# Kernel tuning notes

Measured on AMD Instinct MI355X. Metric: run time of the kernel, lower is better.

Reference implementation:

```python
import jax, jax.numpy as jnp
import numpy as np

CH = 8       # MASK_HEAD.HEAD_CHANNELS
IN_CH = 8    # MASK_BRANCH.OUT_CHANNELS
MASK_OUT_STRIDE = 4
SOI = jnp.array([64.0, 128.0, 256.0, 512.0, 1024.0], dtype=jnp.float32)


def _upsample_ac(x, factor, axis):
    # align_corners=True bilinear upsample along one axis: L -> factor*(L-1)+1
    L = x.shape[axis]
    M = factor * (L - 1) + 1
    pos = jnp.arange(M, dtype=jnp.float32) / factor
    i0 = jnp.floor(pos).astype(jnp.int32)
    i1 = jnp.minimum(i0 + 1, L - 1)
    frac = pos - i0.astype(jnp.float32)
    x0 = jnp.take(x, i0, axis=axis)
    x1 = jnp.take(x, i1, axis=axis)
    sh = [1] * x.ndim
    sh[axis] = M
    frac = frac.reshape(sh)
    return x0 * (1.0 - frac) + x1 * frac


def aligned_bilinear(x, factor):
    # x: [n, 1, H, W] -> [n, 1, factor*H, factor*W] (AdelaiDet aligned_bilinear)
    if factor == 1:
        return x
    h, w = x.shape[2], x.shape[3]
    x = jnp.pad(x, ((0, 0), (0, 0), (0, 1), (0, 1)), mode='edge')
    x = _upsample_ac(x, factor, 2)
    x = _upsample_ac(x, factor, 3)
    p = factor // 2
    x = jnp.pad(x, ((0, 0), (0, 0), (p, 0), (p, 0)), mode='edge')
    return x[:, :, :factor * h, :factor * w]


def setup_inputs() -> dict:
    key = jax.random.key(0)
    k1, k2, k3, k4, k5, k6 = jax.random.split(key, 6)
    N, H, W = 4, 128, 128
    n_inst = 400
    num_gen = (IN_CH + 2) * CH + CH + CH * CH + CH + CH * 1 + 1  # 169
    return {
        'mask_feats': jax.random.normal(k1, (N, IN_CH, H, W), dtype=jnp.float32),
        'mask_shift': jax.random.uniform(k2, (H * W, 2), dtype=jnp.float32),
        'shifts': jax.random.uniform(k3, (n_inst, 2), dtype=jnp.float32),
        'inst_params': jax.random.normal(k4, (n_inst, num_gen), dtype=jnp.float32),
        'im_inds': jax.random.randint(k5, (n_inst,), 0, N, dtype=jnp.int32),
        'fpn_levels': jax.random.randint(k6, (n_inst,), 0, 5, dtype=jnp.int32),
        'mask_feat_stride': 8,
    }


def reference(mask_feats, mask_shift, shifts, inst_params, im_inds, fpn_levels, mask_feat_stride):
    n = inst_params.shape[0]
    N, C, H, W = mask_feats.shape
    # relative coords: [n, 2, H*W]
    rel = shifts[:, None, :] - mask_shift[None, :, :]          # [n, HW, 2]
    rel = jnp.transpose(rel, (0, 2, 1))                        # [n, 2, HW]
    rel = rel / SOI[fpn_levels][:, None, None]
    feats = mask_feats[im_inds].reshape(n, C, H * W)           # [n, C, HW]
    x = jnp.concatenate([rel, feats], axis=1)                  # [n, C+2, HW]
    # parse dynamic params: weights first, then biases
    w1 = inst_params[:, 0:80].reshape(n, CH, IN_CH + 2)
    w2 = inst_params[:, 80:144].reshape(n, CH, CH)
    w3 = inst_params[:, 144:152].reshape(n, 1, CH)
    b1 = inst_params[:, 152:160]
    b2 = inst_params[:, 160:168]
    b3 = inst_params[:, 168:169]
    # per-instance 1x1 convs == batched tiny GEMMs
    x = jax.nn.relu(jnp.einsum('noc,ncp->nop', w1, x) + b1[:, :, None])
    x = jax.nn.relu(jnp.einsum('noc,ncp->nop', w2, x) + b2[:, :, None])
    x = jnp.einsum('noc,ncp->nop', w3, x) + b3[:, :, None]
    logits = x.reshape(n, 1, H, W)
    factor = int(mask_feat_stride) // MASK_OUT_STRIDE
    return aligned_bilinear(logits, factor)
```

## Files before the change

### kernel.cpp

```cpp
#include <hip/hip_runtime.h>


#define HW 16384
#define NP 169

__global__ __launch_bounds__(256)
void pack_kernel(const float* __restrict__ mf, float* __restrict__ rec)
{
    const int g   = blockIdx.x * 256 + threadIdx.x;
    const int img = g >> 14;
    const int p   = g & 16383;
    const float* fb = mf + (size_t)img * 8 * HW + p;
    float4 a = make_float4(fb[0],      fb[HW],     fb[2 * HW], fb[3 * HW]);
    float4 b = make_float4(fb[4 * HW], fb[5 * HW], fb[6 * HW], fb[7 * HW]);
    float4* o = (float4*)(rec + (size_t)g * 8);
    o[0] = a;
    o[1] = b;
}

__global__ __launch_bounds__(256, 6)
void dmh_kernel(const float* __restrict__ mask_feats,
                const float* __restrict__ mask_shift,
                const float* __restrict__ shifts,
                const float* __restrict__ inst_params,
                const int*   __restrict__ im_inds,
                const int*   __restrict__ fpn_levels,
                const float* __restrict__ rec,
                float*       __restrict__ out,
                int use_rec)
{
    __shared__ float lgE[17 * 64];
    __shared__ float lgO[17 * 64];

    const int bx   = blockIdx.x;
    const int inst = bx >> 3;
    const int rg   = bx & 7;
    const int tid  = threadIdx.x;
    const int r0   = rg * 16;

    const int img = im_inds[inst];
    const float* __restrict__ wp = inst_params + (size_t)inst * NP;
    const float s0  = shifts[2 * inst];
    const float s1  = shifts[2 * inst + 1];
    const float inv = 1.0f / (float)(64 << fpn_levels[inst]);
    const float* __restrict__ fb = mask_feats + (size_t)img * 8 * HW;
    const float* __restrict__ rb = rec + (size_t)img * 8 * HW;

    auto load_px = [&](int p, float* x) {
        const int t = p >> 7;
        const int c = p & 127;
        const int r = min(max(r0 - 1 + t, 0), 127);
        const int g = r * 128 + c;
        const float2 ms = *(const float2*)(mask_shift + 2 * g);
        x[0] = (s0 - ms.x) * inv;
        x[1] = (s1 - ms.y) * inv;
        if (use_rec) {
            const float4* q = (const float4*)(rb + (size_t)g * 8);
            const float4 a = q[0], b = q[1];
            x[2] = a.x; x[3] = a.y; x[4] = a.z; x[5] = a.w;
            x[6] = b.x; x[7] = b.y; x[8] = b.z; x[9] = b.w;
        } else {
            #pragma unroll
            for (int k = 0; k < 8; ++k) x[2 + k] = fb[k * HW + g];
        }
    };

    auto store_px = [&](int p, float v) {
        const int t = p >> 7;
        const int c = p & 127;
        const int idx = t * 64 + (c >> 1);
        if (c & 1) lgO[idx] = v; else lgE[idx] = v;
    };

    #pragma unroll
    for (int u = 0; u < 4; ++u) {
        const int pA = tid + 512 * u;
        const int pB = pA + 256;
        float xa[10], xb[10];
        load_px(pA, xa);
        load_px(pB, xb);

        float ya[8], yb[8];
        #pragma unroll
        for (int o = 0; o < 8; ++o) {
            const float bia = wp[152 + o];
            float a = bia, b = bia;
            #pragma unroll
            for (int c = 0; c < 10; ++c) {
                const float w = wp[o * 10 + c];
                a = fmaf(w, xa[c], a);
                b = fmaf(w, xb[c], b);
            }
            ya[o] = fmaxf(a, 0.f);
            yb[o] = fmaxf(b, 0.f);
        }
        float za[8], zb[8];
        #pragma unroll
        for (int o = 0; o < 8; ++o) {
            const float bia = wp[160 + o];
            float a = bia, b = bia;
            #pragma unroll
            for (int c = 0; c < 8; ++c) {
                const float w = wp[80 + o * 8 + c];
                a = fmaf(w, ya[c], a);
                b = fmaf(w, yb[c], b);
            }
            za[o] = fmaxf(a, 0.f);
            zb[o] = fmaxf(b, 0.f);
        }
        float va = wp[168], vb = va;
        #pragma unroll
        for (int c = 0; c < 8; ++c) {
            const float w = wp[144 + c];
            va = fmaf(w, za[c], va);
            vb = fmaf(w, zb[c], vb);
        }
        store_px(pA, va);
        store_px(pB, vb);
    }

    if (tid < 128) {
        const int p = 2048 + tid;
        float x[10];
        load_px(p, x);
        float y1[8];
        #pragma unroll
        for (int o = 0; o < 8; ++o) {
            float a = wp[152 + o];
            #pragma unroll
            for (int c = 0; c < 10; ++c) a = fmaf(wp[o * 10 + c], x[c], a);
            y1[o] = fmaxf(a, 0.f);
        }
        float y2[8];
        #pragma unroll
        for (int o = 0; o < 8; ++o) {
            float a = wp[160 + o];
            #pragma unroll
            for (int c = 0; c < 8; ++c) a = fmaf(wp[80 + o * 8 + c], y1[c], a);
            y2[o] = fmaxf(a, 0.f);
        }
        float v = wp[168];
        #pragma unroll
        for (int c = 0; c < 8; ++c) v = fmaf(wp[144 + c], y2[c], v);
        store_px(p, v);
    }

    __syncthreads();

    float* __restrict__ op =
        out + (size_t)inst * 65536 + (size_t)(2 * r0) * 256;
    const int w = tid >> 6;
    const int l = tid & 63;
    const int parity = w & 1;

    #pragma unroll
    for (int j = 0; j < 8; ++j) {
        const int p2 = (w >> 1) + 2 * j;
        const int yl = 2 * p2 + parity;
        float4 res;
        if (parity) {
            const float* e = lgE + (p2 + 1) * 64;
            const float* o = lgO + (p2 + 1) * 64;
            const float v0 = e[l];
            const float v1 = o[l];
            const float vm = (l > 0) ? o[l - 1] : v0;
            res = make_float4(0.5f * (vm + v0), v0, 0.5f * (v0 + v1), v1);
        } else {
            const float* eA = lgE + p2 * 64;
            const float* oA = lgO + p2 * 64;
            const float* eB = eA + 64;
            const float* oB = oA + 64;
            const float v0A = eA[l], v1A = oA[l];
            const float v0B = eB[l], v1B = oB[l];
            const float vmA = (l > 0) ? oA[l - 1] : v0A;
            const float vmB = (l > 0) ? oB[l - 1] : v0B;
            res = make_float4(0.25f * (vmA + v0A + vmB + v0B),
                              0.5f  * (v0A + v0B),
                              0.25f * (v0A + v1A + v0B + v1B),
                              0.5f  * (v1A + v1B));
        }
        *(float4*)(op + yl * 256 + 4 * l) = res;
    }
}

extern "C" void kernel_launch(void* const* d_in, const int* in_sizes, int n_in,
                              void* d_out, int out_size, void* d_ws, size_t ws_size,
                              hipStream_t stream) {
    (void)n_in; (void)out_size;
    const float* mask_feats  = (const float*)d_in[0];
    const float* mask_shift  = (const float*)d_in[1];
    const float* shifts      = (const float*)d_in[2];
    const float* inst_params = (const float*)d_in[3];
    const int*   im_inds     = (const int*)d_in[4];
    const int*   fpn_levels  = (const int*)d_in[5];
    float* out = (float*)d_out;
    float* rec = (float*)d_ws;

    const int n_inst = in_sizes[2] / 2;
    const size_t rec_bytes = (size_t)4 * HW * 8 * sizeof(float);
    const int use_rec = (ws_size >= rec_bytes) ? 1 : 0;

    if (use_rec)
        pack_kernel<<<dim3(4 * HW / 256), dim3(256), 0, stream>>>(
            mask_feats, rec);

    dmh_kernel<<<dim3(n_inst * 8), dim3(256), 0, stream>>>(
        mask_feats, mask_shift, shifts, inst_params, im_inds, fpn_levels,
        rec, out, use_rec);
}
```

Measured before the change: 152.4 us.

## Drop channel-packing pre-pass and double rows per block to cut halo recompute

Removes the separate pack kernel that reorganised mask features into per-pixel records, so the main kernel reads the channel-planar layout directly with coalesced strided loads. Each block now processes 32 output rows instead of 16, which halves the block count and cuts the duplicated halo-row computation across neighbouring blocks. The trade-off is larger shared memory per block and fewer, longer blocks, which may lower occupancy or load balance. The loop is now only partially unrolled.

```diff
diff --git a/kernel.cpp b/kernel.cpp
--- a/kernel.cpp
+++ b/kernel.cpp
@@ -3,20 +3,6 @@
 
 #define HW 16384
 #define NP 169
-
-__global__ __launch_bounds__(256)
-void pack_kernel(const float* __restrict__ mf, float* __restrict__ rec)
-{
-    const int g   = blockIdx.x * 256 + threadIdx.x;
-    const int img = g >> 14;
-    const int p   = g & 16383;
-    const float* fb = mf + (size_t)img * 8 * HW + p;
-    float4 a = make_float4(fb[0],      fb[HW],     fb[2 * HW], fb[3 * HW]);
-    float4 b = make_float4(fb[4 * HW], fb[5 * HW], fb[6 * HW], fb[7 * HW]);
-    float4* o = (float4*)(rec + (size_t)g * 8);
-    o[0] = a;
-    o[1] = b;
-}
 
 __global__ __launch_bounds__(256, 6)
 void dmh_kernel(const float* __restrict__ mask_feats,
@@ -25,18 +11,16 @@
                 const float* __restrict__ inst_params,
                 const int*   __restrict__ im_inds,
                 const int*   __restrict__ fpn_levels,
-                const float* __restrict__ rec,
-                float*       __restrict__ out,
-                int use_rec)
+                float*       __restrict__ out)
 {
-    __shared__ float lgE[17 * 64];
-    __shared__ float lgO[17 * 64];
+    __shared__ float lgE[33 * 64];
+    __shared__ float lgO[33 * 64];
 
     const int bx   = blockIdx.x;
-    const int inst = bx >> 3;
-    const int rg   = bx & 7;
+    const int inst = bx >> 2;
+    const int rg   = bx & 3;
     const int tid  = threadIdx.x;
-    const int r0   = rg * 16;
+    const int r0   = rg * 32;
 
     const int img = im_inds[inst];
     const float* __restrict__ wp = inst_params + (size_t)inst * NP;
@@ -44,7 +28,6 @@
     const float s1  = shifts[2 * inst + 1];
     const float inv = 1.0f / (float)(64 << fpn_levels[inst]);
     const float* __restrict__ fb = mask_feats + (size_t)img * 8 * HW;
-    const float* __restrict__ rb = rec + (size_t)img * 8 * HW;
 
     auto load_px = [&](int p, float* x) {
         const int t = p >> 7;
@@ -54,15 +37,8 @@
         const float2 ms = *(const float2*)(mask_shift + 2 * g);
         x[0] = (s0 - ms.x) * inv;
         x[1] = (s1 - ms.y) * inv;
-        if (use_rec) {
-            const float4* q = (const float4*)(rb + (size_t)g * 8);
-            const float4 a = q[0], b = q[1];
-            x[2] = a.x; x[3] = a.y; x[4] = a.z; x[5] = a.w;
-            x[6] = b.x; x[7] = b.y; x[8] = b.z; x[9] = b.w;
-        } else {
-            #pragma unroll
-            for (int k = 0; k < 8; ++k) x[2 + k] = fb[k * HW + g];
-        }
+        #pragma unroll
+        for (int k = 0; k < 8; ++k) x[2 + k] = fb[k * HW + g];
     };
 
     auto store_px = [&](int p, float v) {
@@ -72,8 +48,8 @@
         if (c & 1) lgO[idx] = v; else lgE[idx] = v;
     };
 
-    #pragma unroll
-    for (int u = 0; u < 4; ++u) {
+    #pragma unroll 4
+    for (int u = 0; u < 8; ++u) {
         const int pA = tid + 512 * u;
         const int pB = pA + 256;
         float xa[10], xb[10];
@@ -120,7 +96,7 @@
     }
 
     if (tid < 128) {
-        const int p = 2048 + tid;
+        const int p = 4096 + tid;
         float x[10];
         load_px(p, x);
         float y1[8];
@@ -154,7 +130,7 @@
     const int parity = w & 1;
 
     #pragma unroll
-    for (int j = 0; j < 8; ++j) {
+    for (int j = 0; j < 16; ++j) {
         const int p2 = (w >> 1) + 2 * j;
         const int yl = 2 * p2 + parity;
         float4 res;
@@ -186,7 +162,7 @@
 extern "C" void kernel_launch(void* const* d_in, const int* in_sizes, int n_in,
                               void* d_out, int out_size, void* d_ws, size_t ws_size,
                               hipStream_t stream) {
-    (void)n_in; (void)out_size;
+    (void)n_in; (void)out_size; (void)d_ws; (void)ws_size;
     const float* mask_feats  = (const float*)d_in[0];
     const float* mask_shift  = (const float*)d_in[1];
     const float* shifts      = (const float*)d_in[2];
@@ -194,17 +170,10 @@
     const int*   im_inds     = (const int*)d_in[4];
     const int*   fpn_levels  = (const int*)d_in[5];
     float* out = (float*)d_out;
-    float* rec = (float*)d_ws;
 
     const int n_inst = in_sizes[2] / 2;
-    const size_t rec_bytes = (size_t)4 * HW * 8 * sizeof(float);
-    const int use_rec = (ws_size >= rec_bytes) ? 1 : 0;
 
-    if (use_rec)
-        pack_kernel<<<dim3(4 * HW / 256), dim3(256), 0, stream>>>(
-            mask_feats, rec);
-
-    dmh_kernel<<<dim3(n_inst * 8), dim3(256), 0, stream>>>(
+    dmh_kernel<<<dim3(n_inst * 4), dim3(256), 0, stream>>>(
         mask_feats, mask_shift, shifts, inst_params, im_inds, fpn_levels,
-        rec, out, use_rec);
+        out);
 }
```

After: 173.5 us. 1.14x slower.
